# Performance work log

Hardware: AMD Instinct MI355X
Metric: run time of the kernel (lower is better)

## Reference

```python
import jax, jax.numpy as jnp
import numpy as np

N = 1024
IN_FEATURES = 128
N_HEADS = 8
N_HIDDEN = 16  # out_features // n_heads = 128 // 8
NEG_SLOPE = 0.2


def setup_inputs() -> dict:
    key = jax.random.key(0)
    k1, k2, k3, k4, k5 = jax.random.split(key, 5)
    h = jax.random.normal(k1, (N, IN_FEATURES), dtype=jnp.float32)
    adj_mat = jax.random.randint(k2, (N, N, 1), 0, 2, dtype=jnp.int32)
    s = jax.random.normal(k3, (N, N, 1), dtype=jnp.float32)
    # linear: nn.Linear(in_features, n_hidden*n_heads, bias=False) -> weight [128, 128]
    W = jax.random.normal(k4, (N_HEADS * N_HIDDEN, IN_FEATURES), dtype=jnp.float32) * 0.1
    # attn: nn.Linear(2*n_hidden, 1, bias=False) -> weight [1, 32]; stored flat [32]
    attn_w = jax.random.normal(k5, (2 * N_HIDDEN,), dtype=jnp.float32) * 0.1
    return {"h": h, "adj_mat": adj_mat, "s": s, "W": W, "attn_w": attn_w}


def reference(h, adj_mat, s, W, attn_w):
    n_nodes = h.shape[0]
    # g: [N, heads, hidden]
    g = (h @ W.T).reshape(n_nodes, N_HEADS, N_HIDDEN)
    # attn(cat(g_i, g_j)) = a_src . g_i + a_dst . g_j  (linear decomposes over concat)
    a_src = attn_w[:N_HIDDEN]
    a_dst = attn_w[N_HIDDEN:]
    src = jnp.einsum('ihf,f->ih', g, a_src)  # [N, heads]
    dst = jnp.einsum('jhf,f->jh', g, a_dst)  # [N, heads]
    e = jax.nn.leaky_relu(src[:, None, :] + dst[None, :, :], NEG_SLOPE)  # [N, N, heads]
    mask = adj_mat == 0  # [N, N, 1] broadcasts over heads
    neg_inf = jnp.array(-jnp.inf, dtype=e.dtype)
    e = jnp.where(mask, neg_inf, e)
    s_masked = jnp.where(mask, neg_inf, s)  # [N, N, 1]
    a = jax.nn.softmax(e, axis=1)               # [N, N, heads]
    s_prime = jax.nn.softmax(s_masked, axis=1)  # [N, N, 1]
    # NOTE: original applies a third softmax to (a + s_prime) WITHOUT re-masking,
    # so non-edge entries (value 0) get nonzero weight exp(0)/Z — replicated faithfully.
    new_attention = jax.nn.softmax(a + s_prime, axis=1)  # [N, N, heads]
    # dropout is identity in eval mode
    attn_res = jnp.einsum('ijh,jhf->ihf', new_attention, g)  # [N, heads, hidden]
    return attn_res.reshape(n_nodes, N_HEADS * N_HIDDEN)
```

## Files before the change

### kernel.cpp

```cpp
#include <hip/hip_runtime.h>

#define NNODES 1024
#define NHEADS 8
#define NHID 16
#define DIM 128
#define NEG_SLOPE 0.2f

__global__ __launch_bounds__(128) void proj_kernel(
    const float* __restrict__ h, const float* __restrict__ W,
    const float* __restrict__ attn_w,
    float* __restrict__ g, float* __restrict__ srcv, float* __restrict__ dstv)
{
    const int i = blockIdx.x;
    const int o = threadIdx.x;
    __shared__ float hs[DIM];
    hs[o] = h[(size_t)i * DIM + o];
    __syncthreads();
    const float4* hv = (const float4*)hs;
    const float4* wv = (const float4*)(W + (size_t)o * DIM);
    float acc = 0.f;
#pragma unroll
    for (int k = 0; k < DIM / 4; k++) {
        float4 a = hv[k]; float4 b = wv[k];
        acc = fmaf(a.x, b.x, fmaf(a.y, b.y, fmaf(a.z, b.z, fmaf(a.w, b.w, acc))));
    }
    g[(size_t)i * DIM + o] = acc;
    const int f  = o & (NHID - 1);
    const int hd = o >> 4;
    float sv = acc * attn_w[f];
    float dv = acc * attn_w[NHID + f];
#pragma unroll
    for (int off = 8; off > 0; off >>= 1) {
        sv += __shfl_xor(sv, off, 64);
        dv += __shfl_xor(dv, off, 64);
    }
    if (f == 0) { srcv[i * NHEADS + hd] = sv; dstv[i * NHEADS + hd] = dv; }
}

__global__ __launch_bounds__(256, 2) void fused_kernel(
    const int* __restrict__ adj, const float* __restrict__ s,
    const float* __restrict__ g, const float* __restrict__ srcv,
    const float* __restrict__ dstv, float* __restrict__ out)
{
    const int i0   = blockIdx.x * 2;
    const int tid  = threadIdx.x;
    const int lane = tid & 63;
    const int wv   = tid >> 6;
    const int hA   = tid & 7;
    const int jsA  = tid >> 3;
    const int qB   = tid & 3;
    const int hB   = (tid >> 2) & 7;
    const int jsB  = tid >> 5;

    __shared__ float evL[2][NNODES];
    __shared__ float dstL[NNODES * NHEADS];
    __shared__ float sh_src[2][NHEADS];
    __shared__ float zeA[4][NHEADS][2];
    __shared__ float zsA[4][2];
    __shared__ float statE[2][NHEADS];
    __shared__ float statS[2];
    __shared__ float redO[4][2][NHEADS][4][4];
    __shared__ float ztA[4][2][NHEADS];

    float zs[2] = {0.f, 0.f};
#pragma unroll
    for (int r = 0; r < 2; r++) {
        const int4   a  = ((const int4*)  adj)[(size_t)(i0 + r) * (NNODES/4) + tid];
        const float4 sv = ((const float4*)s  )[(size_t)(i0 + r) * (NNODES/4) + tid];
        float4 e4;
        e4.x = a.x ? __expf(sv.x) : 0.f;
        e4.y = a.y ? __expf(sv.y) : 0.f;
        e4.z = a.z ? __expf(sv.z) : 0.f;
        e4.w = a.w ? __expf(sv.w) : 0.f;
        ((float4*)evL[r])[tid] = e4;
        zs[r] += e4.x + e4.y + e4.z + e4.w;
    }
    {
        const float4* dv4 = (const float4*)dstv;
        float4* dl4 = (float4*)dstL;
#pragma unroll
        for (int k = 0; k < 8; k++) dl4[k * 256 + tid] = dv4[k * 256 + tid];
        if (tid < 16) sh_src[tid >> 3][tid & 7] =
            srcv[(size_t)(i0 + (tid >> 3)) * NHEADS + (tid & 7)];
    }
    __syncthreads();

    float ze[2] = {0.f, 0.f};
    {
        const float sHA[2] = { sh_src[0][hA], sh_src[1][hA] };
#pragma unroll 4
        for (int t = 0; t < 32; t++) {
            const int j = t * 32 + jsA;
            const float d = dstL[j * NHEADS + hA];
#pragma unroll
            for (int r = 0; r < 2; r++) {
                float e = sHA[r] + d;
                e = e > 0.f ? e : NEG_SLOPE * e;
                const float x = __expf(e);
                ze[r] += (evL[r][j] != 0.f) ? x : 0.f;
            }
        }
    }
#pragma unroll
    for (int off = 8; off <= 32; off <<= 1)
#pragma unroll
        for (int r = 0; r < 2; r++) ze[r] += __shfl_xor(ze[r], off, 64);
#pragma unroll
    for (int off = 1; off <= 32; off <<= 1)
#pragma unroll
        for (int r = 0; r < 2; r++) zs[r] += __shfl_xor(zs[r], off, 64);
    if (lane < NHEADS) { zeA[wv][lane][0] = ze[0]; zeA[wv][lane][1] = ze[1]; }
    if (lane == 0)     { zsA[wv][0] = zs[0]; zsA[wv][1] = zs[1]; }
    __syncthreads();
    if (tid < 16) {
        const int hh = tid & 7, rr = tid >> 3;
        statE[rr][hh] = 1.f / (zeA[0][hh][rr] + zeA[1][hh][rr] +
                               zeA[2][hh][rr] + zeA[3][hh][rr]);
    } else if (tid < 18) {
        const int rr = tid - 16;
        statS[rr] = 1.f / (zsA[0][rr] + zsA[1][rr] + zsA[2][rr] + zsA[3][rr]);
    }
    __syncthreads();

    const float ize[2] = { statE[0][hB], statE[1][hB] };
    const float izs[2] = { statS[0],     statS[1]     };
    const float sHB[2] = { sh_src[0][hB], sh_src[1][hB] };
    const int   base   = lane & ~3;

    float acc[2][4] = {{0.f,0.f,0.f,0.f},{0.f,0.f,0.f,0.f}};
    float zt[2] = {0.f, 0.f};
    const float4* g4 = (const float4*)g;

#pragma unroll 2
    for (int tg = 0; tg < 32; tg++) {
        const int jw = (tg * 4 + qB) * 8 + jsB;
        const float d = dstL[jw * NHEADS + hB];
        float w[2];
#pragma unroll
        for (int r = 0; r < 2; r++) {
            float e = sHB[r] + d;
            e = e > 0.f ? e : NEG_SLOPE * e;
            const float x  = __expf(e);
            const float ev = evL[r][jw];
            const float arg = (ev != 0.f) ? fmaf(x, ize[r], ev * izs[r]) : 0.f;
            w[r] = __expf(arg);
            zt[r] += w[r];
        }
#pragma unroll
        for (int k = 0; k < 4; k++) {
            const int j = (tg * 4 + k) * 8 + jsB;
            const float4 gv = g4[(size_t)j * 32 + hB * 4 + qB];
            const float w0 = __shfl(w[0], base + k, 64);
            const float w1 = __shfl(w[1], base + k, 64);
            acc[0][0] = fmaf(w0, gv.x, acc[0][0]);
            acc[0][1] = fmaf(w0, gv.y, acc[0][1]);
            acc[0][2] = fmaf(w0, gv.z, acc[0][2]);
            acc[0][3] = fmaf(w0, gv.w, acc[0][3]);
            acc[1][0] = fmaf(w1, gv.x, acc[1][0]);
            acc[1][1] = fmaf(w1, gv.y, acc[1][1]);
            acc[1][2] = fmaf(w1, gv.z, acc[1][2]);
            acc[1][3] = fmaf(w1, gv.w, acc[1][3]);
        }
    }

#pragma unroll
    for (int r = 0; r < 2; r++)
#pragma unroll
        for (int m = 0; m < 4; m++) acc[r][m] += __shfl_xor(acc[r][m], 32, 64);
#pragma unroll
    for (int r = 0; r < 2; r++) {
        zt[r] += __shfl_xor(zt[r], 1, 64);
        zt[r] += __shfl_xor(zt[r], 2, 64);
        zt[r] += __shfl_xor(zt[r], 32, 64);
    }
    if (lane < 32) {
#pragma unroll
        for (int r = 0; r < 2; r++)
            *(float4*)&redO[wv][r][hB][qB][0] =
                make_float4(acc[r][0], acc[r][1], acc[r][2], acc[r][3]);
        if ((lane & 3) == 0) { ztA[wv][0][hB] = zt[0]; ztA[wv][1][hB] = zt[1]; }
    }
    __syncthreads();
    {
        const int rr = tid >> 7;
        const int hf = tid & 127;
        const int oh = hf >> 4;
        const int qq = (hf >> 2) & 3;
        const int mm = hf & 3;
        const float v  = redO[0][rr][oh][qq][mm] + redO[1][rr][oh][qq][mm] +
                         redO[2][rr][oh][qq][mm] + redO[3][rr][oh][qq][mm];
        const float zq = ztA[0][rr][oh] + ztA[1][rr][oh] +
                         ztA[2][rr][oh] + ztA[3][rr][oh];
        out[(size_t)(i0 + rr) * DIM + hf] = v / zq;
    }
}

extern "C" void kernel_launch(void* const* d_in, const int* in_sizes, int n_in,
                              void* d_out, int out_size, void* d_ws, size_t ws_size,
                              hipStream_t stream) {
    const float* h      = (const float*)d_in[0];
    const int*   adj    = (const int*)  d_in[1];
    const float* s      = (const float*)d_in[2];
    const float* W      = (const float*)d_in[3];
    const float* attn_w = (const float*)d_in[4];
    float* out = (float*)d_out;

    float* g    = (float*)d_ws;
    float* srcv = g    + (size_t)NNODES * DIM;
    float* dstv = srcv + (size_t)NNODES * NHEADS;

    proj_kernel <<<NNODES, DIM, 0, stream>>>(h, W, attn_w, g, srcv, dstv);
    fused_kernel<<<NNODES / 2, 256, 0, stream>>>(adj, s, g, srcv, dstv, out);
}
```

Baseline: 87.31 us.

## Tile projection through shared memory and double fused-kernel block size with DPP broadcasts

```diff
diff --git a/kernel.cpp b/kernel.cpp
--- a/kernel.cpp
+++ b/kernel.cpp
@@ -6,38 +6,54 @@
 #define DIM 128
 #define NEG_SLOPE 0.2f
 
-__global__ __launch_bounds__(128) void proj_kernel(
+template<int CTRL>
+__device__ __forceinline__ float qbcast(float v) {
+    return __int_as_float(__builtin_amdgcn_mov_dpp(__float_as_int(v), CTRL, 0xF, 0xF, true));
+}
+
+__global__ __launch_bounds__(256) void proj_kernel(
     const float* __restrict__ h, const float* __restrict__ W,
     const float* __restrict__ attn_w,
     float* __restrict__ g, float* __restrict__ srcv, float* __restrict__ dstv)
 {
-    const int i = blockIdx.x;
-    const int o = threadIdx.x;
-    __shared__ float hs[DIM];
-    hs[o] = h[(size_t)i * DIM + o];
-    __syncthreads();
-    const float4* hv = (const float4*)hs;
-    const float4* wv = (const float4*)(W + (size_t)o * DIM);
+    const int bi = blockIdx.x & 63;
+    const int bh = blockIdx.x >> 6;
+    const int i0 = bi << 4;
+    const int tid = threadIdx.x;
+    __shared__ float4 hs[16][33];
+    __shared__ float4 ws[16][33];
+    const float4* h4 = (const float4*)h;
+    const float4* W4 = (const float4*)W;
+    {
+        const int t0 = tid, t1 = tid + 256;
+        hs[t0 >> 5][t0 & 31] = h4[(size_t)i0 * 32 + t0];
+        hs[t1 >> 5][t1 & 31] = h4[(size_t)i0 * 32 + t1];
+        ws[t0 >> 5][t0 & 31] = W4[(size_t)(bh * 16) * 32 + t0];
+        ws[t1 >> 5][t1 & 31] = W4[(size_t)(bh * 16) * 32 + t1];
+    }
+    __syncthreads();
+    const int il = tid >> 4;
+    const int f  = tid & 15;
     float acc = 0.f;
 #pragma unroll
-    for (int k = 0; k < DIM / 4; k++) {
-        float4 a = hv[k]; float4 b = wv[k];
+    for (int k = 0; k < 32; k++) {
+        const float4 a = hs[il][k];
+        const float4 b = ws[f][k];
         acc = fmaf(a.x, b.x, fmaf(a.y, b.y, fmaf(a.z, b.z, fmaf(a.w, b.w, acc))));
     }
-    g[(size_t)i * DIM + o] = acc;
-    const int f  = o & (NHID - 1);
-    const int hd = o >> 4;
+    const int i = i0 + il;
+    g[(size_t)i * DIM + bh * NHID + f] = acc;
     float sv = acc * attn_w[f];
     float dv = acc * attn_w[NHID + f];
 #pragma unroll
-    for (int off = 8; off > 0; off >>= 1) {
+    for (int off = 1; off <= 8; off <<= 1) {
         sv += __shfl_xor(sv, off, 64);
         dv += __shfl_xor(dv, off, 64);
     }
-    if (f == 0) { srcv[i * NHEADS + hd] = sv; dstv[i * NHEADS + hd] = dv; }
-}
-
-__global__ __launch_bounds__(256, 2) void fused_kernel(
+    if (f == 0) { srcv[i * NHEADS + bh] = sv; dstv[i * NHEADS + bh] = dv; }
+}
+
+__global__ __launch_bounds__(512, 4) void fused_kernel(
     const int* __restrict__ adj, const float* __restrict__ s,
     const float* __restrict__ g, const float* __restrict__ srcv,
     const float* __restrict__ dstv, float* __restrict__ out)
@@ -46,152 +62,152 @@
     const int tid  = threadIdx.x;
     const int lane = tid & 63;
     const int wv   = tid >> 6;
-    const int hA   = tid & 7;
-    const int jsA  = tid >> 3;
-    const int qB   = tid & 3;
-    const int hB   = (tid >> 2) & 7;
-    const int jsB  = tid >> 5;
 
     __shared__ float evL[2][NNODES];
     __shared__ float dstL[NNODES * NHEADS];
     __shared__ float sh_src[2][NHEADS];
-    __shared__ float zeA[4][NHEADS][2];
-    __shared__ float zsA[4][2];
+    __shared__ float zeA[8][NHEADS][2];
+    __shared__ float zsA[8];
     __shared__ float statE[2][NHEADS];
     __shared__ float statS[2];
-    __shared__ float redO[4][2][NHEADS][4][4];
-    __shared__ float ztA[4][2][NHEADS];
-
-    float zs[2] = {0.f, 0.f};
-#pragma unroll
-    for (int r = 0; r < 2; r++) {
-        const int4   a  = ((const int4*)  adj)[(size_t)(i0 + r) * (NNODES/4) + tid];
-        const float4 sv = ((const float4*)s  )[(size_t)(i0 + r) * (NNODES/4) + tid];
+    __shared__ float redO[8][2][NHEADS][4][4];
+    __shared__ float ztA[8][2][NHEADS];
+
+    const int rA = tid >> 8;
+    const int cA = tid & 255;
+    float zs;
+    {
+        const int4   a  = ((const int4*)  adj)[(size_t)(i0 + rA) * (NNODES/4) + cA];
+        const float4 sv = ((const float4*)s  )[(size_t)(i0 + rA) * (NNODES/4) + cA];
         float4 e4;
         e4.x = a.x ? __expf(sv.x) : 0.f;
         e4.y = a.y ? __expf(sv.y) : 0.f;
         e4.z = a.z ? __expf(sv.z) : 0.f;
         e4.w = a.w ? __expf(sv.w) : 0.f;
-        ((float4*)evL[r])[tid] = e4;
-        zs[r] += e4.x + e4.y + e4.z + e4.w;
+        ((float4*)evL[rA])[cA] = e4;
+        zs = e4.x + e4.y + e4.z + e4.w;
     }
     {
         const float4* dv4 = (const float4*)dstv;
         float4* dl4 = (float4*)dstL;
 #pragma unroll
-        for (int k = 0; k < 8; k++) dl4[k * 256 + tid] = dv4[k * 256 + tid];
+        for (int k = 0; k < 4; k++) dl4[k * 512 + tid] = dv4[k * 512 + tid];
         if (tid < 16) sh_src[tid >> 3][tid & 7] =
             srcv[(size_t)(i0 + (tid >> 3)) * NHEADS + (tid & 7)];
     }
-    __syncthreads();
-
-    float ze[2] = {0.f, 0.f};
-    {
-        const float sHA[2] = { sh_src[0][hA], sh_src[1][hA] };
+#pragma unroll
+    for (int off = 1; off <= 32; off <<= 1) zs += __shfl_xor(zs, off, 64);
+    if (lane == 0) zsA[wv] = zs;
+    __syncthreads();
+
+    const int hA  = tid & 7;
+    const int jsA = tid >> 3;
+    float ze0 = 0.f, ze1 = 0.f;
+    {
+        const float sH0 = sh_src[0][hA], sH1 = sh_src[1][hA];
 #pragma unroll 4
-        for (int t = 0; t < 32; t++) {
-            const int j = t * 32 + jsA;
+        for (int t = 0; t < 16; t++) {
+            const int j = t * 64 + jsA;
             const float d = dstL[j * NHEADS + hA];
-#pragma unroll
-            for (int r = 0; r < 2; r++) {
-                float e = sHA[r] + d;
-                e = e > 0.f ? e : NEG_SLOPE * e;
-                const float x = __expf(e);
-                ze[r] += (evL[r][j] != 0.f) ? x : 0.f;
-            }
+            float e0 = sH0 + d; e0 = e0 > 0.f ? e0 : NEG_SLOPE * e0;
+            float e1 = sH1 + d; e1 = e1 > 0.f ? e1 : NEG_SLOPE * e1;
+            ze0 += (evL[0][j] != 0.f) ? __expf(e0) : 0.f;
+            ze1 += (evL[1][j] != 0.f) ? __expf(e1) : 0.f;
         }
     }
 #pragma unroll
-    for (int off = 8; off <= 32; off <<= 1)
-#pragma unroll
-        for (int r = 0; r < 2; r++) ze[r] += __shfl_xor(ze[r], off, 64);
-#pragma unroll
-    for (int off = 1; off <= 32; off <<= 1)
-#pragma unroll
-        for (int r = 0; r < 2; r++) zs[r] += __shfl_xor(zs[r], off, 64);
-    if (lane < NHEADS) { zeA[wv][lane][0] = ze[0]; zeA[wv][lane][1] = ze[1]; }
-    if (lane == 0)     { zsA[wv][0] = zs[0]; zsA[wv][1] = zs[1]; }
+    for (int off = 8; off <= 32; off <<= 1) {
+        ze0 += __shfl_xor(ze0, off, 64);
+        ze1 += __shfl_xor(ze1, off, 64);
+    }
+    if (lane < NHEADS) { zeA[wv][lane][0] = ze0; zeA[wv][lane][1] = ze1; }
     __syncthreads();
     if (tid < 16) {
         const int hh = tid & 7, rr = tid >> 3;
-        statE[rr][hh] = 1.f / (zeA[0][hh][rr] + zeA[1][hh][rr] +
-                               zeA[2][hh][rr] + zeA[3][hh][rr]);
+        float z = 0.f;
+#pragma unroll
+        for (int w2 = 0; w2 < 8; w2++) z += zeA[w2][hh][rr];
+        statE[rr][hh] = 1.f / z;
     } else if (tid < 18) {
         const int rr = tid - 16;
-        statS[rr] = 1.f / (zsA[0][rr] + zsA[1][rr] + zsA[2][rr] + zsA[3][rr]);
-    }
-    __syncthreads();
-
-    const float ize[2] = { statE[0][hB], statE[1][hB] };
-    const float izs[2] = { statS[0],     statS[1]     };
-    const float sHB[2] = { sh_src[0][hB], sh_src[1][hB] };
-    const int   base   = lane & ~3;
-
-    float acc[2][4] = {{0.f,0.f,0.f,0.f},{0.f,0.f,0.f,0.f}};
-    float zt[2] = {0.f, 0.f};
+        statS[rr] = 1.f / (zsA[rr*4] + zsA[rr*4+1] + zsA[rr*4+2] + zsA[rr*4+3]);
+    }
+    __syncthreads();
+
+    const int qB  = tid & 3;
+    const int hB  = (tid >> 2) & 7;
+    const int jsB = tid >> 5;
+    const float ize0 = statE[0][hB], ize1 = statE[1][hB];
+    const float izs0 = statS[0],     izs1 = statS[1];
+    const float sB0  = sh_src[0][hB], sB1 = sh_src[1][hB];
+
+    float acc0[4] = {0.f,0.f,0.f,0.f};
+    float acc1[4] = {0.f,0.f,0.f,0.f};
+    float zt0 = 0.f, zt1 = 0.f;
     const float4* g4 = (const float4*)g;
+    const int jw0   = qB * 16 + jsB;
+    const int gidx0 = jsB * 32 + hB * 4 + qB;
 
 #pragma unroll 2
-    for (int tg = 0; tg < 32; tg++) {
-        const int jw = (tg * 4 + qB) * 8 + jsB;
+    for (int tg = 0; tg < 16; tg++) {
+        const int jw = tg * 64 + jw0;
         const float d = dstL[jw * NHEADS + hB];
-        float w[2];
-#pragma unroll
-        for (int r = 0; r < 2; r++) {
-            float e = sHB[r] + d;
-            e = e > 0.f ? e : NEG_SLOPE * e;
-            const float x  = __expf(e);
-            const float ev = evL[r][jw];
-            const float arg = (ev != 0.f) ? fmaf(x, ize[r], ev * izs[r]) : 0.f;
-            w[r] = __expf(arg);
-            zt[r] += w[r];
+        float e0 = sB0 + d; e0 = e0 > 0.f ? e0 : NEG_SLOPE * e0;
+        float e1 = sB1 + d; e1 = e1 > 0.f ? e1 : NEG_SLOPE * e1;
+        const float x0 = __expf(e0), x1 = __expf(e1);
+        const float ev0 = evL[0][jw], ev1 = evL[1][jw];
+        const float a0 = (ev0 != 0.f) ? fmaf(x0, ize0, ev0 * izs0) : 0.f;
+        const float a1 = (ev1 != 0.f) ? fmaf(x1, ize1, ev1 * izs1) : 0.f;
+        const float w0 = __expf(a0), w1 = __expf(a1);
+        zt0 += w0; zt1 += w1;
+
+#define KSTEP(K, CTRL)                                                        \
+        {                                                                     \
+            const float w0k = qbcast<CTRL>(w0);                               \
+            const float w1k = qbcast<CTRL>(w1);                               \
+            const float4 gv = g4[gidx0 + tg * 2048 + (K) * 512];              \
+            acc0[0] = fmaf(w0k, gv.x, acc0[0]);                               \
+            acc0[1] = fmaf(w0k, gv.y, acc0[1]);                               \
+            acc0[2] = fmaf(w0k, gv.z, acc0[2]);                               \
+            acc0[3] = fmaf(w0k, gv.w, acc0[3]);                               \
+            acc1[0] = fmaf(w1k, gv.x, acc1[0]);                               \
+            acc1[1] = fmaf(w1k, gv.y, acc1[1]);                               \
+            acc1[2] = fmaf(w1k, gv.z, acc1[2]);                               \
+            acc1[3] = fmaf(w1k, gv.w, acc1[3]);                               \
         }
-#pragma unroll
-        for (int k = 0; k < 4; k++) {
-            const int j = (tg * 4 + k) * 8 + jsB;
-            const float4 gv = g4[(size_t)j * 32 + hB * 4 + qB];
-            const float w0 = __shfl(w[0], base + k, 64);
-            const float w1 = __shfl(w[1], base + k, 64);
-            acc[0][0] = fmaf(w0, gv.x, acc[0][0]);
-            acc[0][1] = fmaf(w0, gv.y, acc[0][1]);
-            acc[0][2] = fmaf(w0, gv.z, acc[0][2]);
-            acc[0][3] = fmaf(w0, gv.w, acc[0][3]);
-            acc[1][0] = fmaf(w1, gv.x, acc[1][0]);
-            acc[1][1] = fmaf(w1, gv.y, acc[1][1]);
-            acc[1][2] = fmaf(w1, gv.z, acc[1][2]);
-            acc[1][3] = fmaf(w1, gv.w, acc[1][3]);
-        }
-    }
-
-#pragma unroll
-    for (int r = 0; r < 2; r++)
-#pragma unroll
-        for (int m = 0; m < 4; m++) acc[r][m] += __shfl_xor(acc[r][m], 32, 64);
-#pragma unroll
-    for (int r = 0; r < 2; r++) {
-        zt[r] += __shfl_xor(zt[r], 1, 64);
-        zt[r] += __shfl_xor(zt[r], 2, 64);
-        zt[r] += __shfl_xor(zt[r], 32, 64);
-    }
+        KSTEP(0, 0x00)
+        KSTEP(1, 0x55)
+        KSTEP(2, 0xAA)
+        KSTEP(3, 0xFF)
+#undef KSTEP
+    }
+
+#pragma unroll
+    for (int m = 0; m < 4; m++) {
+        acc0[m] += __shfl_xor(acc0[m], 32, 64);
+        acc1[m] += __shfl_xor(acc1[m], 32, 64);
+    }
+    zt0 += __shfl_xor(zt0, 1, 64); zt0 += __shfl_xor(zt0, 2, 64); zt0 += __shfl_xor(zt0, 32, 64);
+    zt1 += __shfl_xor(zt1, 1, 64); zt1 += __shfl_xor(zt1, 2, 64); zt1 += __shfl_xor(zt1, 32, 64);
     if (lane < 32) {
-#pragma unroll
-        for (int r = 0; r < 2; r++)
-            *(float4*)&redO[wv][r][hB][qB][0] =
-                make_float4(acc[r][0], acc[r][1], acc[r][2], acc[r][3]);
-        if ((lane & 3) == 0) { ztA[wv][0][hB] = zt[0]; ztA[wv][1][hB] = zt[1]; }
-    }
-    __syncthreads();
-    {
+        *(float4*)&redO[wv][0][hB][qB][0] = make_float4(acc0[0], acc0[1], acc0[2], acc0[3]);
+        *(float4*)&redO[wv][1][hB][qB][0] = make_float4(acc1[0], acc1[1], acc1[2], acc1[3]);
+        if ((lane & 3) == 0) { ztA[wv][0][hB] = zt0; ztA[wv][1][hB] = zt1; }
+    }
+    __syncthreads();
+    if (tid < 256) {
         const int rr = tid >> 7;
         const int hf = tid & 127;
         const int oh = hf >> 4;
         const int qq = (hf >> 2) & 3;
         const int mm = hf & 3;
-        const float v  = redO[0][rr][oh][qq][mm] + redO[1][rr][oh][qq][mm] +
-                         redO[2][rr][oh][qq][mm] + redO[3][rr][oh][qq][mm];
-        const float zq = ztA[0][rr][oh] + ztA[1][rr][oh] +
-                         ztA[2][rr][oh] + ztA[3][rr][oh];
-        out[(size_t)(i0 + rr) * DIM + hf] = v / zq;
+        float v = 0.f, z = 0.f;
+#pragma unroll
+        for (int w2 = 0; w2 < 8; w2++) {
+            v += redO[w2][rr][oh][qq][mm];
+            z += ztA[w2][rr][oh];
+        }
+        out[(size_t)(i0 + rr) * DIM + hf] = v / z;
     }
 }
 
@@ -209,6 +225,6 @@
     float* srcv = g    + (size_t)NNODES * DIM;
     float* dstv = srcv + (size_t)NNODES * NHEADS;
 
-    proj_kernel <<<NNODES, DIM, 0, stream>>>(h, W, attn_w, g, srcv, dstv);
-    fused_kernel<<<NNODES / 2, 256, 0, stream>>>(adj, s, g, srcv, dstv, out);
-}
+    proj_kernel <<<512, 256, 0, stream>>>(h, W, attn_w, g, srcv, dstv);
+    fused_kernel<<<NNODES / 2, 512, 0, stream>>>(adj, s, g, srcv, dstv, out);
+}
```

Result: faster. 80.70 us (-7.6%).
